# Kernel optimization log

Hardware: AMD Instinct MI355X
Metric: run time of the kernel (lower is better)

The kernel has to match this reference:

```python
import jax, jax.numpy as jnp
import numpy as np

N = 500_000
K = 16
E = N * K
H = 256


def _linear_params(key, fan_in, fan_out):
    k1, k2 = jax.random.split(key)
    bound = 1.0 / np.sqrt(fan_in)
    W = jax.random.uniform(k1, (fan_in, fan_out), jnp.float32, -bound, bound)
    b = jax.random.uniform(k2, (fan_out,), jnp.float32, -bound, bound)
    return W, b


def setup_inputs() -> dict:
    key = jax.random.key(0)
    ks = jax.random.split(key, 10)
    x = jax.random.normal(ks[0], (N, 3), jnp.float32)
    edge_index = jax.random.randint(ks[1], (2, E), 0, N, jnp.int64)
    edge_attr = jax.random.normal(ks[2], (E, 1), jnp.float32)
    W1, b1 = _linear_params(ks[3], K, H)          # GNN1 message MLP: Linear(k, 256)
    We1, be1 = _linear_params(ks[4], H, 128)      # encoder Linear(256,128)
    We2, be2 = _linear_params(ks[5], 128, 6)      # encoder Linear(128,6)
    Wd1, bd1 = _linear_params(ks[6], 6, 128)      # decoder Linear(6,128)
    Wd2, bd2 = _linear_params(ks[7], 128, H)      # decoder Linear(128,256)
    Wo, bo = _linear_params(ks[8], H, 1)          # output Linear(256,1)
    return {"x": x, "edge_index": edge_index, "edge_attr": edge_attr,
            "W1": W1, "b1": b1, "We1": We1, "be1": be1, "We2": We2, "be2": be2,
            "Wd1": Wd1, "bd1": bd1, "Wd2": Wd2, "bd2": bd2, "Wo": Wo, "bo": bo}


def reference(x, edge_index, edge_attr, W1, b1, We1, be1, We2, be2,
              Wd1, bd1, Wd2, bd2, Wo, bo):
    # GNN1: messages are edge_attr verbatim (x_i/x_j ignored); aggregate reshapes
    # all E scalar messages into (N, k) (k edges per node, contiguous) and runs
    # Linear(k,256)+Tanh. Note: LSTM and GCN4 branches in the torch code are dead
    # (GNN1 ignores its node-feature input), so they do not affect the output.
    k = W1.shape[0]
    msgs = edge_attr.reshape(-1, k)                    # (N, k)
    h = jnp.tanh(msgs @ W1 + b1)                       # (N, 256)
    # second L1 call produces the identical result (depends only on edge_attr)
    z = jnp.tanh(jnp.tanh(h @ We1 + be1) @ We2 + be2)  # encoder -> (N, 6)
    d = jnp.tanh(z @ Wd1 + bd1) @ Wd2 + bd2            # decoder -> (N, 256)
    out = jax.nn.sigmoid(jnp.tanh(d) @ Wo + bo)        # (N, 1)
    return out[:, 0]                                   # squeeze(dim=1) -> (N,)
```

## Files before the change

### kernel.cpp

```cpp
#include <hip/hip_runtime.h>


#define N_NODES 500000

#define OFF_W1 0
#define OFF_W2 8192
#define OFF_W3 73728
#define OFF_W4 77824
#define OFF_W5 86016
#define OFF_WO 151552
#define OFF_B1 152576
#define OFF_B2 153600
#define OFF_B3 154112
#define OFF_B4 154176
#define OFF_B5 154688
#define IMG_BYTES 155712
#define IMG_ALLOC 156672

#define K1_LDS   79872
#define K1_B1    77824
#define K1_B2    78848
#define K1_B3    79360
#define K2_LDS   76800
#define K2_W4    0
#define K2_W5    8192
#define K2_WO    73728
#define K2_B4    74752
#define K2_B5    75264

typedef _Float16 half8  __attribute__((ext_vector_type(8)));
typedef __fp16   pk16x2 __attribute__((ext_vector_type(2)));
typedef float    f32x4  __attribute__((ext_vector_type(4)));
typedef int      int4v  __attribute__((ext_vector_type(4)));

__device__ __align__(16) char g_img[IMG_ALLOC];

static __device__ __forceinline__ unsigned pack_f16_rne(float a, float b) {
  _Float16 ha = (_Float16)a, hb = (_Float16)b;
  unsigned short ua = __builtin_bit_cast(unsigned short, ha);
  unsigned short ub = __builtin_bit_cast(unsigned short, hb);
  return (unsigned)ua | ((unsigned)ub << 16);
}
static __device__ __forceinline__ int pkrtz(float a, float b) {
  pk16x2 h = __builtin_amdgcn_cvt_pkrtz(a, b);
  return __builtin_bit_cast(int, h);
}
static __device__ __forceinline__ float tanh_f(float x) {
  float e = __builtin_amdgcn_exp2f(x * 2.8853900817779268f);
  float r = __builtin_amdgcn_rcpf(e + 1.0f);
  return __builtin_fmaf(-2.0f, r, 1.0f);
}
static __device__ __forceinline__ float sigmoid_f(float x) {
  float e = __builtin_amdgcn_exp2f(x * -1.4426950408889634f);
  return __builtin_amdgcn_rcpf(1.0f + e);
}
static __device__ __forceinline__ f32x4 mfma16(half8 a, int4v b, f32x4 c) {
  return __builtin_amdgcn_mfma_f32_16x16x32_f16(a, __builtin_bit_cast(half8, b), c, 0, 0, 0);
}
static __device__ __forceinline__ half8 lda(const char* smem, int off) {
  return *(const half8*)(smem + off);
}
static __device__ __forceinline__ f32x4 ldf4(const char* smem, int off) {
  return *(const f32x4*)(smem + off);
}
#define FENCE() __builtin_amdgcn_sched_barrier(0)

struct PK2 { int lo, hi; };
static __device__ __forceinline__ PK2 tp(f32x4 a) {
  PK2 p;
  p.lo = pkrtz(tanh_f(a.x), tanh_f(a.y));
  p.hi = pkrtz(tanh_f(a.z), tanh_f(a.w));
  return p;
}

__global__ void gnn_prep(const float* __restrict__ W1,  const float* __restrict__ b1,
                         const float* __restrict__ We1, const float* __restrict__ be1,
                         const float* __restrict__ We2, const float* __restrict__ be2,
                         const float* __restrict__ Wd1, const float* __restrict__ bd1,
                         const float* __restrict__ Wd2, const float* __restrict__ bd2,
                         const float* __restrict__ Wo)
{
  int t = blockIdx.x * 256 + threadIdx.x;
  int off = t * 4;
  if (off >= IMG_BYTES) return;
  unsigned val;
  if (off < OFF_W2) {
    int rel = off;
    int mi = rel >> 9, li = (rel >> 4) & 31, j2 = (rel >> 2) & 3;
    int fout = mi * 16 + (li & 15);
    int k0 = (li >> 4) * 8 + j2 * 2;
    val = pack_f16_rne(W1[k0 * 256 + fout], W1[(k0 + 1) * 256 + fout]);
  } else if (off < OFF_W3) {
    int rel = off - OFF_W2;
    int blk = rel >> 10, li = (rel >> 4) & 63, j2 = (rel >> 2) & 3;
    int mi = blk >> 3, ki = blk & 7;
    int fout = mi * 16 + (li & 15);
    int k0 = ki * 32 + 4 * (li >> 4) + 16 * (j2 >> 1) + 2 * (j2 & 1);
    val = pack_f16_rne(We1[k0 * 128 + fout], We1[(k0 + 1) * 128 + fout]);
  } else if (off < OFF_W4) {
    int rel = off - OFF_W3;
    int ki = rel >> 10, li = (rel >> 4) & 63, j2 = (rel >> 2) & 3;
    int fo = li & 15;
    int k0 = ki * 32 + 4 * (li >> 4) + 16 * (j2 >> 1) + 2 * (j2 & 1);
    float a = (fo < 6) ? We2[k0 * 6 + fo] : 0.0f;
    float b = (fo < 6) ? We2[(k0 + 1) * 6 + fo] : 0.0f;
    val = pack_f16_rne(a, b);
  } else if (off < OFF_W5) {
    int rel = off - OFF_W4;
    int mi = rel >> 10, li = (rel >> 4) & 63, j2 = (rel >> 2) & 3;
    int fout = mi * 16 + (li & 15);
    int qa = li >> 4;
    unsigned v = 0;
    if (j2 < 2) {
      int k0 = 4 * qa + 2 * j2;
      float a = (k0 < 6)     ? Wd1[k0 * 128 + fout]       : 0.0f;
      float b = (k0 + 1 < 6) ? Wd1[(k0 + 1) * 128 + fout] : 0.0f;
      v = pack_f16_rne(a, b);
    }
    val = v;
  } else if (off < OFF_WO) {
    int rel = off - OFF_W5;
    int blk = rel >> 10, li = (rel >> 4) & 63, j2 = (rel >> 2) & 3;
    int mi = blk >> 2, ki = blk & 3;
    int fout = mi * 16 + (li & 15);
    int k0 = ki * 32 + 4 * (li >> 4) + 16 * (j2 >> 1) + 2 * (j2 & 1);
    val = pack_f16_rne(Wd2[k0 * 256 + fout], Wd2[(k0 + 1) * 256 + fout]);
  } else if (off < OFF_B1) {
    val = __builtin_bit_cast(unsigned, Wo[(off - OFF_WO) >> 2]);
  } else if (off < OFF_B2) {
    val = __builtin_bit_cast(unsigned, b1[(off - OFF_B1) >> 2]);
  } else if (off < OFF_B3) {
    val = __builtin_bit_cast(unsigned, be1[(off - OFF_B2) >> 2]);
  } else if (off < OFF_B4) {
    int i = (off - OFF_B3) >> 2;
    float v = (i < 6) ? be2[i] : 0.0f;
    val = __builtin_bit_cast(unsigned, v);
  } else if (off < OFF_B5) {
    val = __builtin_bit_cast(unsigned, bd1[(off - OFF_B4) >> 2]);
  } else {
    val = __builtin_bit_cast(unsigned, bd2[(off - OFF_B5) >> 2]);
  }
  *(unsigned*)(g_img + off) = val;
}

static __device__ __forceinline__ void stage_chunk(const char* src, char* dst) {
  __builtin_amdgcn_global_load_lds(
      (const __attribute__((address_space(1))) void*)src,
      (__attribute__((address_space(3))) void*)dst, 16, 0, 0);
}

#define L1_PAIR(KO, OUT_G0, OUT_G1) do {                                   \
    half8 Ae = lda(smem, OFF_W1 + (2*(KO))*512 + (ln & 31)*16);            \
    half8 Ao = lda(smem, OFF_W1 + (2*(KO)+1)*512 + (ln & 31)*16);          \
    if (!qlo) { Ae = h8z; Ao = h8z; }                                      \
    f32x4 be_ = ldf4(smem, K1_B1 + (2*(KO))*64 + q*16);                    \
    f32x4 bo_ = ldf4(smem, K1_B1 + (2*(KO)+1)*64 + q*16);                  \
    f32x4 ae0 = mfma16(Ae, b1g0, be_);                                     \
    f32x4 ae1 = mfma16(Ae, b1g1, be_);                                     \
    f32x4 ao0 = mfma16(Ao, b1g0, bo_);                                     \
    f32x4 ao1 = mfma16(Ao, b1g1, bo_);                                     \
    PK2 pe0 = tp(ae0), po0 = tp(ao0), pe1 = tp(ae1), po1 = tp(ao1);        \
    OUT_G0.x = pe0.lo; OUT_G0.y = pe0.hi; OUT_G0.z = po0.lo; OUT_G0.w = po0.hi; \
    OUT_G1.x = pe1.lo; OUT_G1.y = pe1.hi; OUT_G1.z = po1.lo; OUT_G1.w = po1.hi; \
    FENCE();                                                               \
  } while (0)

#define L2_MI(MI, ACC0, ACC1) do {                                                            \
    f32x4 bb = ldf4(smem, K1_B2 + (MI)*64 + q*16);                                            \
    ACC0 = bb; ACC1 = bb;                                                                     \
    half8 A;                                                                                  \
    A = lda(smem, OFF_W2 + ((MI)*8+0)*1024 + ln*16); ACC0 = mfma16(A, c2g0_0, ACC0); ACC1 = mfma16(A, c2g1_0, ACC1); \
    A = lda(smem, OFF_W2 + ((MI)*8+1)*1024 + ln*16); ACC0 = mfma16(A, c2g0_1, ACC0); ACC1 = mfma16(A, c2g1_1, ACC1); \
    A = lda(smem, OFF_W2 + ((MI)*8+2)*1024 + ln*16); ACC0 = mfma16(A, c2g0_2, ACC0); ACC1 = mfma16(A, c2g1_2, ACC1); \
    A = lda(smem, OFF_W2 + ((MI)*8+3)*1024 + ln*16); ACC0 = mfma16(A, c2g0_3, ACC0); ACC1 = mfma16(A, c2g1_3, ACC1); \
    A = lda(smem, OFF_W2 + ((MI)*8+4)*1024 + ln*16); ACC0 = mfma16(A, c2g0_4, ACC0); ACC1 = mfma16(A, c2g1_4, ACC1); \
    A = lda(smem, OFF_W2 + ((MI)*8+5)*1024 + ln*16); ACC0 = mfma16(A, c2g0_5, ACC0); ACC1 = mfma16(A, c2g1_5, ACC1); \
    A = lda(smem, OFF_W2 + ((MI)*8+6)*1024 + ln*16); ACC0 = mfma16(A, c2g0_6, ACC0); ACC1 = mfma16(A, c2g1_6, ACC1); \
    A = lda(smem, OFF_W2 + ((MI)*8+7)*1024 + ln*16); ACC0 = mfma16(A, c2g0_7, ACC0); ACC1 = mfma16(A, c2g1_7, ACC1); \
  } while (0)

#define L2_PAIR(KO, OUT_G0, OUT_G1) do {                                   \
    f32x4 ve0, ve1, vo0, vo1;                                              \
    L2_MI(2*(KO),   ve0, ve1);                                             \
    FENCE();                                                               \
    L2_MI(2*(KO)+1, vo0, vo1);                                             \
    PK2 pe0 = tp(ve0), po0 = tp(vo0), pe1 = tp(ve1), po1 = tp(vo1);        \
    OUT_G0.x = pe0.lo; OUT_G0.y = pe0.hi; OUT_G0.z = po0.lo; OUT_G0.w = po0.hi; \
    OUT_G1.x = pe1.lo; OUT_G1.y = pe1.hi; OUT_G1.z = po1.lo; OUT_G1.w = po1.hi; \
    FENCE();                                                               \
  } while (0)

__global__ __launch_bounds__(512)
void gnn_k1(const float* __restrict__ ea, int4v* __restrict__ zbuf)
{
  __shared__ __align__(16) char smem[K1_LDS];
  const int tid = threadIdx.x;
  const int wv = tid >> 6, ln = tid & 63;

#pragma unroll 1
  for (int r = 0; r < 10; ++r) {
    int cb = (r * 8 + wv) << 6;
    if (cb < 4992) {
      int src = (cb < 4864) ? cb * 16 : OFF_B1 + (cb - 4864) * 16;
      stage_chunk(g_img + src + ln * 16, smem + (size_t)cb * 16 + ln * 16);
    }
  }
  __syncthreads();

  const int q = ln >> 4, c = ln & 15;
  const bool qlo = (q < 2);
  const int4v zi4 = {0, 0, 0, 0};
  const half8 h8z = __builtin_bit_cast(half8, zi4);

  const int NT = (N_NODES + 255) / 256;
#pragma unroll 1
  for (int t = blockIdx.x; t < NT; t += gridDim.x) {
    const int base = t * 256 + wv * 32;

    int nl = base + (q >> 1) * 16 + c;
    if (nl > N_NODES - 1) nl = N_NODES - 1;
    const f32x4* ea4 = (const f32x4*)ea;
    size_t eb = (size_t)nl * 4 + (size_t)((q & 1) * 2);
    f32x4 vlo = ea4[eb];
    f32x4 vhi = ea4[eb + 1];
    int p0 = pkrtz(vlo.x, vlo.y), p1 = pkrtz(vlo.z, vlo.w);
    int p2 = pkrtz(vhi.x, vhi.y), p3 = pkrtz(vhi.z, vhi.w);
    int4v b1g0, b1g1;
    b1g0.x = qlo ? p0 : 0; b1g0.y = qlo ? p1 : 0;
    b1g0.z = qlo ? p2 : 0; b1g0.w = qlo ? p3 : 0;
    int sh = (ln + 32) & 63;
    int r0 = __shfl(p0, sh, 64), r1 = __shfl(p1, sh, 64);
    int r2 = __shfl(p2, sh, 64), r3 = __shfl(p3, sh, 64);
    b1g1.x = qlo ? r0 : 0; b1g1.y = qlo ? r1 : 0;
    b1g1.z = qlo ? r2 : 0; b1g1.w = qlo ? r3 : 0;

    int4v c2g0_0, c2g0_1, c2g0_2, c2g0_3, c2g0_4, c2g0_5, c2g0_6, c2g0_7;
    int4v c2g1_0, c2g1_1, c2g1_2, c2g1_3, c2g1_4, c2g1_5, c2g1_6, c2g1_7;
    L1_PAIR(0, c2g0_0, c2g1_0);
    L1_PAIR(1, c2g0_1, c2g1_1);
    L1_PAIR(2, c2g0_2, c2g1_2);
    L1_PAIR(3, c2g0_3, c2g1_3);
    L1_PAIR(4, c2g0_4, c2g1_4);
    L1_PAIR(5, c2g0_5, c2g1_5);
    L1_PAIR(6, c2g0_6, c2g1_6);
    L1_PAIR(7, c2g0_7, c2g1_7);

    int4v c3g0_0, c3g0_1, c3g0_2, c3g0_3;
    int4v c3g1_0, c3g1_1, c3g1_2, c3g1_3;
    L2_PAIR(0, c3g0_0, c3g1_0);
    L2_PAIR(1, c3g0_1, c3g1_1);
    L2_PAIR(2, c3g0_2, c3g1_2);
    L2_PAIR(3, c3g0_3, c3g1_3);

    f32x4 bb3 = ldf4(smem, K1_B3 + q * 16);
    f32x4 z0 = bb3, z1 = bb3;
    half8 A;
    A = lda(smem, OFF_W3 + 0 * 1024 + ln * 16); z0 = mfma16(A, c3g0_0, z0); z1 = mfma16(A, c3g1_0, z1);
    A = lda(smem, OFF_W3 + 1 * 1024 + ln * 16); z0 = mfma16(A, c3g0_1, z0); z1 = mfma16(A, c3g1_1, z1);
    A = lda(smem, OFF_W3 + 2 * 1024 + ln * 16); z0 = mfma16(A, c3g0_2, z0); z1 = mfma16(A, c3g1_2, z1);
    A = lda(smem, OFF_W3 + 3 * 1024 + ln * 16); z0 = mfma16(A, c3g0_3, z0); z1 = mfma16(A, c3g1_3, z1);
    PK2 p3g0 = tp(z0);
    PK2 p3g1 = tp(z1);

    if (ln < 32) {
      int4v zv;
      zv.x = p3g0.lo; zv.y = p3g0.hi; zv.z = p3g1.lo; zv.w = p3g1.hi;
      zbuf[(size_t)(t * 8 + wv) * 32 + ln] = zv;
    }
  }
}

#define L4_MI(MI, ACC0, ACC1) do {                                         \
    f32x4 bb = ldf4(smem, K2_B4 + (MI)*64 + q*16);                         \
    half8 A = lda(smem, K2_W4 + (MI)*1024 + ln*16);                        \
    ACC0 = mfma16(A, b4g0, bb);                                            \
    ACC1 = mfma16(A, b4g1, bb);                                            \
  } while (0)

#define L4_PAIR(KO, OUT_G0, OUT_G1) do {                                   \
    f32x4 ve0, ve1, vo0, vo1;                                              \
    L4_MI(2*(KO),   ve0, ve1);                                             \
    L4_MI(2*(KO)+1, vo0, vo1);                                             \
    PK2 pe0 = tp(ve0), po0 = tp(vo0), pe1 = tp(ve1), po1 = tp(vo1);        \
    OUT_G0.x = pe0.lo; OUT_G0.y = pe0.hi; OUT_G0.z = po0.lo; OUT_G0.w = po0.hi; \
    OUT_G1.x = pe1.lo; OUT_G1.y = pe1.hi; OUT_G1.z = po1.lo; OUT_G1.w = po1.hi; \
    FENCE();                                                               \
  } while (0)

#define L5_MI(MI) do {                                                                        \
    f32x4 bb = ldf4(smem, K2_B5 + (MI)*64 + q*16);                                            \
    f32x4 a0 = bb, a1 = bb;                                                                   \
    half8 A;                                                                                  \
    A = lda(smem, K2_W5 + ((MI)*4+0)*1024 + ln*16); a0 = mfma16(A, c5g0_0, a0); a1 = mfma16(A, c5g1_0, a1); \
    A = lda(smem, K2_W5 + ((MI)*4+1)*1024 + ln*16); a0 = mfma16(A, c5g0_1, a0); a1 = mfma16(A, c5g1_1, a1); \
    A = lda(smem, K2_W5 + ((MI)*4+2)*1024 + ln*16); a0 = mfma16(A, c5g0_2, a0); a1 = mfma16(A, c5g1_2, a1); \
    A = lda(smem, K2_W5 + ((MI)*4+3)*1024 + ln*16); a0 = mfma16(A, c5g0_3, a0); a1 = mfma16(A, c5g1_3, a1); \
    f32x4 wo = ldf4(smem, K2_WO + (MI)*64 + q*16);                                            \
    part0 += tanh_f(a0.x)*wo.x + tanh_f(a0.y)*wo.y + tanh_f(a0.z)*wo.z + tanh_f(a0.w)*wo.w;   \
    part1 += tanh_f(a1.x)*wo.x + tanh_f(a1.y)*wo.y + tanh_f(a1.z)*wo.z + tanh_f(a1.w)*wo.w;   \
    FENCE();                                                                                  \
  } while (0)

__global__ __launch_bounds__(512)
void gnn_k2(const int4v* __restrict__ zbuf, float* __restrict__ out,
            const float* __restrict__ bo_p)
{
  __shared__ __align__(16) char smem[K2_LDS];
  const int tid = threadIdx.x;
  const int wv = tid >> 6, ln = tid & 63;

#pragma unroll 1
  for (int r = 0; r < 10; ++r) {
    int cb = (r * 8 + wv) << 6;
    if (cb < 4800) {
      int src;
      if (cb < 512)       src = OFF_W4 + cb * 16;
      else if (cb < 4672) src = OFF_W5 + (cb - 512) * 16;
      else                src = OFF_B4 + (cb - 4672) * 16;
      stage_chunk(g_img + src + ln * 16, smem + (size_t)cb * 16 + ln * 16);
    }
  }
  __syncthreads();

  const int q = ln >> 4, c = ln & 15;
  const float bo = *bo_p;

  const int NT = (N_NODES + 255) / 256;
#pragma unroll 1
  for (int t = blockIdx.x; t < NT; t += gridDim.x) {
    const int base = t * 256 + wv * 32;

    int4v zv = {0, 0, 0, 0};
    if (ln < 32) zv = zbuf[(size_t)(t * 8 + wv) * 32 + ln];

    int4v b4g0, b4g1;
    b4g0.x = zv.x; b4g0.y = zv.y; b4g0.z = 0; b4g0.w = 0;
    b4g1.x = zv.z; b4g1.y = zv.w; b4g1.z = 0; b4g1.w = 0;

    int4v c5g0_0, c5g0_1, c5g0_2, c5g0_3;
    int4v c5g1_0, c5g1_1, c5g1_2, c5g1_3;
    L4_PAIR(0, c5g0_0, c5g1_0);
    L4_PAIR(1, c5g0_1, c5g1_1);
    L4_PAIR(2, c5g0_2, c5g1_2);
    L4_PAIR(3, c5g0_3, c5g1_3);

    float part0 = 0.0f, part1 = 0.0f;
    L5_MI(0);  L5_MI(1);  L5_MI(2);  L5_MI(3);
    L5_MI(4);  L5_MI(5);  L5_MI(6);  L5_MI(7);
    L5_MI(8);  L5_MI(9);  L5_MI(10); L5_MI(11);
    L5_MI(12); L5_MI(13); L5_MI(14); L5_MI(15);

    part0 += __shfl_xor(part0, 16, 64); part0 += __shfl_xor(part0, 32, 64);
    part1 += __shfl_xor(part1, 16, 64); part1 += __shfl_xor(part1, 32, 64);
    if (q < 2) {
      int node = base + q * 16 + c;
      if (node < N_NODES) {
        float v = ((q == 0) ? part0 : part1) + bo;
        out[node] = sigmoid_f(v);
      }
    }
  }
}

extern "C" void kernel_launch(void* const* d_in, const int* in_sizes, int n_in,
                              void* d_out, int out_size, void* d_ws, size_t ws_size,
                              hipStream_t stream) {
  (void)in_sizes; (void)n_in; (void)ws_size; (void)out_size;
  const float* ea  = (const float*)d_in[2];
  const float* W1  = (const float*)d_in[3];
  const float* b1  = (const float*)d_in[4];
  const float* We1 = (const float*)d_in[5];
  const float* be1 = (const float*)d_in[6];
  const float* We2 = (const float*)d_in[7];
  const float* be2 = (const float*)d_in[8];
  const float* Wd1 = (const float*)d_in[9];
  const float* bd1 = (const float*)d_in[10];
  const float* Wd2 = (const float*)d_in[11];
  const float* bd2 = (const float*)d_in[12];
  const float* Wo  = (const float*)d_in[13];
  const float* bo  = (const float*)d_in[14];

  gnn_prep<<<dim3((IMG_BYTES / 4 + 255) / 256), dim3(256), 0, stream>>>(
      W1, b1, We1, be1, We2, be2, Wd1, bd1, Wd2, bd2, Wo);
  gnn_k1<<<dim3(512), dim3(512), 0, stream>>>(ea, (int4v*)d_ws);
  gnn_k2<<<dim3(512), dim3(512), 0, stream>>>((const int4v*)d_ws, (float*)d_out, bo);
}
```

Before: 249.3 us.

## Fold tanh scaling into weights so activations become bare sigmoid

Rewrites tanh(x) as 1-2*sigmoid(2x) and folds the scale factors and the 1-2s affine into the prepacked weights and biases. Each activation becomes exp2 plus rcp, dropping a multiply and an FMA per element across all layers, and the output bias is adjusted to absorb Wo's sum. It also replaces the per-lane zeroing of the L1 A/B operands with address selection into a zero LDS region. This adds precision risk, since weights are scaled by about -5.77 before the fp16 conversion and the sigmoid outputs lie in [0,1] instead of [-1,1].

New measurement: 241.2 us. 1.03x faster.

```diff
diff --git a/kernel.cpp b/kernel.cpp
--- a/kernel.cpp
+++ b/kernel.cpp
@@ -14,13 +14,16 @@
 #define OFF_B3 154112
 #define OFF_B4 154176
 #define OFF_B5 154688
-#define IMG_BYTES 155712
+#define OFF_EXTRA 155712
+#define OFF_ZERO  155728
+#define IMG_END   156240
 #define IMG_ALLOC 156672
 
-#define K1_LDS   79872
 #define K1_B1    77824
 #define K1_B2    78848
 #define K1_B3    79360
+#define K1_Z     79872
+#define K1_LDS   80384
 #define K2_LDS   76800
 #define K2_W4    0
 #define K2_W5    8192
@@ -28,6 +31,8 @@
 #define K2_B4    74752
 #define K2_B5    75264
 
+#define SCONST (-2.8853900817779268f)
+
 typedef _Float16 half8  __attribute__((ext_vector_type(8)));
 typedef __fp16   pk16x2 __attribute__((ext_vector_type(2)));
 typedef float    f32x4  __attribute__((ext_vector_type(4)));
@@ -45,10 +50,9 @@
   pk16x2 h = __builtin_amdgcn_cvt_pkrtz(a, b);
   return __builtin_bit_cast(int, h);
 }
-static __device__ __forceinline__ float tanh_f(float x) {
-  float e = __builtin_amdgcn_exp2f(x * 2.8853900817779268f);
-  float r = __builtin_amdgcn_rcpf(e + 1.0f);
-  return __builtin_fmaf(-2.0f, r, 1.0f);
+static __device__ __forceinline__ float sig2(float y) {
+  float e = __builtin_amdgcn_exp2f(y);
+  return __builtin_amdgcn_rcpf(1.0f + e);
 }
 static __device__ __forceinline__ float sigmoid_f(float x) {
   float e = __builtin_amdgcn_exp2f(x * -1.4426950408889634f);
@@ -68,8 +72,8 @@
 struct PK2 { int lo, hi; };
 static __device__ __forceinline__ PK2 tp(f32x4 a) {
   PK2 p;
-  p.lo = pkrtz(tanh_f(a.x), tanh_f(a.y));
-  p.hi = pkrtz(tanh_f(a.z), tanh_f(a.w));
+  p.lo = pkrtz(sig2(a.x), sig2(a.y));
+  p.hi = pkrtz(sig2(a.z), sig2(a.w));
   return p;
 }
 
@@ -78,32 +82,33 @@
                          const float* __restrict__ We2, const float* __restrict__ be2,
                          const float* __restrict__ Wd1, const float* __restrict__ bd1,
                          const float* __restrict__ Wd2, const float* __restrict__ bd2,
-                         const float* __restrict__ Wo)
+                         const float* __restrict__ Wo,  const float* __restrict__ bo)
 {
   int t = blockIdx.x * 256 + threadIdx.x;
   int off = t * 4;
-  if (off >= IMG_BYTES) return;
+  if (off >= IMG_END) return;
   unsigned val;
   if (off < OFF_W2) {
     int rel = off;
     int mi = rel >> 9, li = (rel >> 4) & 31, j2 = (rel >> 2) & 3;
     int fout = mi * 16 + (li & 15);
     int k0 = (li >> 4) * 8 + j2 * 2;
-    val = pack_f16_rne(W1[k0 * 256 + fout], W1[(k0 + 1) * 256 + fout]);
+    val = pack_f16_rne(SCONST * W1[k0 * 256 + fout], SCONST * W1[(k0 + 1) * 256 + fout]);
   } else if (off < OFF_W3) {
     int rel = off - OFF_W2;
     int blk = rel >> 10, li = (rel >> 4) & 63, j2 = (rel >> 2) & 3;
     int mi = blk >> 3, ki = blk & 7;
     int fout = mi * 16 + (li & 15);
     int k0 = ki * 32 + 4 * (li >> 4) + 16 * (j2 >> 1) + 2 * (j2 & 1);
-    val = pack_f16_rne(We1[k0 * 128 + fout], We1[(k0 + 1) * 128 + fout]);
+    val = pack_f16_rne(2.0f * SCONST * We1[k0 * 128 + fout],
+                       2.0f * SCONST * We1[(k0 + 1) * 128 + fout]);
   } else if (off < OFF_W4) {
     int rel = off - OFF_W3;
     int ki = rel >> 10, li = (rel >> 4) & 63, j2 = (rel >> 2) & 3;
     int fo = li & 15;
     int k0 = ki * 32 + 4 * (li >> 4) + 16 * (j2 >> 1) + 2 * (j2 & 1);
-    float a = (fo < 6) ? We2[k0 * 6 + fo] : 0.0f;
-    float b = (fo < 6) ? We2[(k0 + 1) * 6 + fo] : 0.0f;
+    float a = (fo < 6) ? 2.0f * SCONST * We2[k0 * 6 + fo] : 0.0f;
+    float b = (fo < 6) ? 2.0f * SCONST * We2[(k0 + 1) * 6 + fo] : 0.0f;
     val = pack_f16_rne(a, b);
   } else if (off < OFF_W5) {
     int rel = off - OFF_W4;
@@ -113,8 +118,8 @@
     unsigned v = 0;
     if (j2 < 2) {
       int k0 = 4 * qa + 2 * j2;
-      float a = (k0 < 6)     ? Wd1[k0 * 128 + fout]       : 0.0f;
-      float b = (k0 + 1 < 6) ? Wd1[(k0 + 1) * 128 + fout] : 0.0f;
+      float a = (k0 < 6)     ? 2.0f * SCONST * Wd1[k0 * 128 + fout]       : 0.0f;
+      float b = (k0 + 1 < 6) ? 2.0f * SCONST * Wd1[(k0 + 1) * 128 + fout] : 0.0f;
       v = pack_f16_rne(a, b);
     }
     val = v;
@@ -124,21 +129,42 @@
     int mi = blk >> 2, ki = blk & 3;
     int fout = mi * 16 + (li & 15);
     int k0 = ki * 32 + 4 * (li >> 4) + 16 * (j2 >> 1) + 2 * (j2 & 1);
-    val = pack_f16_rne(Wd2[k0 * 256 + fout], Wd2[(k0 + 1) * 256 + fout]);
+    val = pack_f16_rne(2.0f * SCONST * Wd2[k0 * 256 + fout],
+                       2.0f * SCONST * Wd2[(k0 + 1) * 256 + fout]);
   } else if (off < OFF_B1) {
-    val = __builtin_bit_cast(unsigned, Wo[(off - OFF_WO) >> 2]);
+    val = __builtin_bit_cast(unsigned, 2.0f * Wo[(off - OFF_WO) >> 2]);
   } else if (off < OFF_B2) {
-    val = __builtin_bit_cast(unsigned, b1[(off - OFF_B1) >> 2]);
+    val = __builtin_bit_cast(unsigned, SCONST * b1[(off - OFF_B1) >> 2]);
   } else if (off < OFF_B3) {
-    val = __builtin_bit_cast(unsigned, be1[(off - OFF_B2) >> 2]);
+    int i = (off - OFF_B2) >> 2;
+    float s = 0.0f;
+    for (int k = 0; k < 256; ++k) s += We1[k * 128 + i];
+    val = __builtin_bit_cast(unsigned, SCONST * (be1[i] - s));
   } else if (off < OFF_B4) {
     int i = (off - OFF_B3) >> 2;
-    float v = (i < 6) ? be2[i] : 0.0f;
+    float v = 0.0f;
+    if (i < 6) {
+      float s = 0.0f;
+      for (int k = 0; k < 128; ++k) s += We2[k * 6 + i];
+      v = SCONST * (be2[i] - s);
+    }
     val = __builtin_bit_cast(unsigned, v);
   } else if (off < OFF_B5) {
-    val = __builtin_bit_cast(unsigned, bd1[(off - OFF_B4) >> 2]);
+    int i = (off - OFF_B4) >> 2;
+    float s = 0.0f;
+    for (int k = 0; k < 6; ++k) s += Wd1[k * 128 + i];
+    val = __builtin_bit_cast(unsigned, SCONST * (bd1[i] - s));
+  } else if (off < OFF_EXTRA) {
+    int i = (off - OFF_B5) >> 2;
+    float s = 0.0f;
+    for (int k = 0; k < 128; ++k) s += Wd2[k * 256 + i];
+    val = __builtin_bit_cast(unsigned, SCONST * (bd2[i] - s));
+  } else if (off == OFF_EXTRA) {
+    float s = 0.0f;
+    for (int k = 0; k < 256; ++k) s += Wo[k];
+    val = __builtin_bit_cast(unsigned, bo[0] - s);
   } else {
-    val = __builtin_bit_cast(unsigned, bd2[(off - OFF_B5) >> 2]);
+    val = 0;
   }
   *(unsigned*)(g_img + off) = val;
 }
@@ -150,9 +176,8 @@
 }
 
 #define L1_PAIR(KO, OUT_G0, OUT_G1) do {                                   \
-    half8 Ae = lda(smem, OFF_W1 + (2*(KO))*512 + (ln & 31)*16);            \
-    half8 Ao = lda(smem, OFF_W1 + (2*(KO)+1)*512 + (ln & 31)*16);          \
-    if (!qlo) { Ae = h8z; Ao = h8z; }                                      \
+    half8 Ae = lda(smem, w1b + (2*(KO))*w1s);                              \
+    half8 Ao = lda(smem, w1b + (2*(KO)+1)*w1s);                            \
     f32x4 be_ = ldf4(smem, K1_B1 + (2*(KO))*64 + q*16);                    \
     f32x4 bo_ = ldf4(smem, K1_B1 + (2*(KO)+1)*64 + q*16);                  \
     f32x4 ae0 = mfma16(Ae, b1g0, be_);                                     \
@@ -200,8 +225,11 @@
 #pragma unroll 1
   for (int r = 0; r < 10; ++r) {
     int cb = (r * 8 + wv) << 6;
-    if (cb < 4992) {
-      int src = (cb < 4864) ? cb * 16 : OFF_B1 + (cb - 4864) * 16;
+    if (cb < 5024) {
+      int src;
+      if (cb < 4864)      src = cb * 16;
+      else if (cb < 4992) src = OFF_B1 + (cb - 4864) * 16;
+      else                src = OFF_ZERO + (cb - 4992) * 16;
       stage_chunk(g_img + src + ln * 16, smem + (size_t)cb * 16 + ln * 16);
     }
   }
@@ -209,8 +237,9 @@
 
   const int q = ln >> 4, c = ln & 15;
   const bool qlo = (q < 2);
-  const int4v zi4 = {0, 0, 0, 0};
-  const half8 h8z = __builtin_bit_cast(half8, zi4);
+  const int lnl16 = (ln & 31) * 16;
+  const int w1b = qlo ? (OFF_W1 + lnl16) : (K1_Z + lnl16);
+  const int w1s = qlo ? 512 : 0;
 
   const int NT = (N_NODES + 255) / 256;
 #pragma unroll 1
@@ -223,16 +252,13 @@
     size_t eb = (size_t)nl * 4 + (size_t)((q & 1) * 2);
     f32x4 vlo = ea4[eb];
     f32x4 vhi = ea4[eb + 1];
-    int p0 = pkrtz(vlo.x, vlo.y), p1 = pkrtz(vlo.z, vlo.w);
-    int p2 = pkrtz(vhi.x, vhi.y), p3 = pkrtz(vhi.z, vhi.w);
-    int4v b1g0, b1g1;
-    b1g0.x = qlo ? p0 : 0; b1g0.y = qlo ? p1 : 0;
-    b1g0.z = qlo ? p2 : 0; b1g0.w = qlo ? p3 : 0;
+    int4v b1g0;
+    b1g0.x = pkrtz(vlo.x, vlo.y); b1g0.y = pkrtz(vlo.z, vlo.w);
+    b1g0.z = pkrtz(vhi.x, vhi.y); b1g0.w = pkrtz(vhi.z, vhi.w);
     int sh = (ln + 32) & 63;
-    int r0 = __shfl(p0, sh, 64), r1 = __shfl(p1, sh, 64);
-    int r2 = __shfl(p2, sh, 64), r3 = __shfl(p3, sh, 64);
-    b1g1.x = qlo ? r0 : 0; b1g1.y = qlo ? r1 : 0;
-    b1g1.z = qlo ? r2 : 0; b1g1.w = qlo ? r3 : 0;
+    int4v b1g1;
+    b1g1.x = __shfl(b1g0.x, sh, 64); b1g1.y = __shfl(b1g0.y, sh, 64);
+    b1g1.z = __shfl(b1g0.z, sh, 64); b1g1.w = __shfl(b1g0.w, sh, 64);
 
     int4v c2g0_0, c2g0_1, c2g0_2, c2g0_3, c2g0_4, c2g0_5, c2g0_6, c2g0_7;
     int4v c2g1_0, c2g1_1, c2g1_2, c2g1_3, c2g1_4, c2g1_5, c2g1_6, c2g1_7;
@@ -296,14 +322,13 @@
     A = lda(smem, K2_W5 + ((MI)*4+2)*1024 + ln*16); a0 = mfma16(A, c5g0_2, a0); a1 = mfma16(A, c5g1_2, a1); \
     A = lda(smem, K2_W5 + ((MI)*4+3)*1024 + ln*16); a0 = mfma16(A, c5g0_3, a0); a1 = mfma16(A, c5g1_3, a1); \
     f32x4 wo = ldf4(smem, K2_WO + (MI)*64 + q*16);                                            \
-    part0 += tanh_f(a0.x)*wo.x + tanh_f(a0.y)*wo.y + tanh_f(a0.z)*wo.z + tanh_f(a0.w)*wo.w;   \
-    part1 += tanh_f(a1.x)*wo.x + tanh_f(a1.y)*wo.y + tanh_f(a1.z)*wo.z + tanh_f(a1.w)*wo.w;   \
+    part0 += sig2(a0.x)*wo.x + sig2(a0.y)*wo.y + sig2(a0.z)*wo.z + sig2(a0.w)*wo.w;           \
+    part1 += sig2(a1.x)*wo.x + sig2(a1.y)*wo.y + sig2(a1.z)*wo.z + sig2(a1.w)*wo.w;           \
     FENCE();                                                                                  \
   } while (0)
 
 __global__ __launch_bounds__(512)
-void gnn_k2(const int4v* __restrict__ zbuf, float* __restrict__ out,
-            const float* __restrict__ bo_p)
+void gnn_k2(const int4v* __restrict__ zbuf, float* __restrict__ out)
 {
   __shared__ __align__(16) char smem[K2_LDS];
   const int tid = threadIdx.x;
@@ -323,7 +348,7 @@
   __syncthreads();
 
   const int q = ln >> 4, c = ln & 15;
-  const float bo = *bo_p;
+  const float bo2 = *(const float*)(g_img + OFF_EXTRA);
 
   const int NT = (N_NODES + 255) / 256;
 #pragma unroll 1
@@ -355,7 +380,7 @@
     if (q < 2) {
       int node = base + q * 16 + c;
       if (node < N_NODES) {
-        float v = ((q == 0) ? part0 : part1) + bo;
+        float v = ((q == 0) ? part0 : part1) + bo2;
         out[node] = sigmoid_f(v);
       }
     }
@@ -380,8 +405,8 @@
   const float* Wo  = (const float*)d_in[13];
   const float* bo  = (const float*)d_in[14];
 
-  gnn_prep<<<dim3((IMG_BYTES / 4 + 255) / 256), dim3(256), 0, stream>>>(
-      W1, b1, We1, be1, We2, be2, Wd1, bd1, Wd2, bd2, Wo);
+  gnn_prep<<<dim3((IMG_END / 4 + 255) / 256), dim3(256), 0, stream>>>(
+      W1, b1, We1, be1, We2, be2, Wd1, bd1, Wd2, bd2, Wo, bo);
   gnn_k1<<<dim3(512), dim3(512), 0, stream>>>(ea, (int4v*)d_ws);
-  gnn_k2<<<dim3(512), dim3(512), 0, stream>>>((const int4v*)d_ws, (float*)d_out, bo);
-}
+  gnn_k2<<<dim3(512), dim3(512), 0, stream>>>((const int4v*)d_ws, (float*)d_out);
+}
```
